# Optimization experiments

Measured on AMD Instinct MI355X. Metric: run time of the kernel, lower is better.

## Reference

```python
import jax, jax.numpy as jnp
import numpy as np
from jax import lax

B, C, H, W = 16, 512, 16, 300
K, G = 8, 2          # k_clusters, g_clusters (gvlad)
OUT = 5994           # n speakers
DN = ('NCHW', 'OIHW', 'NCHW')


def setup_inputs() -> dict:
    key = jax.random.key(0)
    ks = jax.random.split(key, 10)
    s = lambda fan: 1.0 / np.sqrt(fan)
    return {
        'x5': jax.random.normal(ks[0], (B, C, H, W), jnp.float32),
        'x4': jnp.zeros((1, 1, 1, 1), jnp.float32),
        'x3': jnp.zeros((1, 1, 1, 1), jnp.float32),
        'x2': jnp.zeros((1, 1, 1, 1), jnp.float32),
        'x1': jnp.zeros((1, 1, 1, 1), jnp.float32),
        'conv_w': jax.random.normal(ks[1], (C, C, 7, 1), jnp.float32) * s(C * 7),
        'conv_b': jnp.zeros((C,), jnp.float32),
        'cc_w': jax.random.normal(ks[2], (K + G, C, 7, 1), jnp.float32) * s(C * 7),
        'cc_b': jnp.zeros((K + G,), jnp.float32),
        'centroids': jax.random.normal(ks[3], (K + G, C), jnp.float32),
        'fc_w': jax.random.normal(ks[4], (C, C * K), jnp.float32) * s(C * K),
        'fc_b': jnp.zeros((C,), jnp.float32),
        'logit_w': jax.random.normal(ks[5], (OUT, C), jnp.float32) * s(C),
    }


def _conv(x, w, b=None):
    y = lax.conv_general_dilated(x, w, (1, 1), 'VALID', dimension_numbers=DN)
    if b is not None:
        y = y + b[None, :, None, None]
    return y


def _forward(x5, conv_w, conv_b, cc_w, cc_b, centroids, fc_w, fc_b, logit_w):
    feats = jnp.maximum(_conv(x5, conv_w, conv_b), 0.0)      # (B,C,H',W) relu conv
    scores = _conv(x5, cc_w, cc_b)                           # (B,K+G,H',W)
    assign = jax.nn.softmax(scores, axis=1)                  # soft cluster assignment
    # VLAD: sum_hw a[b,k,h,w]*(f[b,c,h,w] - cent[k,c]), computed without
    # materializing the (B,K+G,C,H',W) residual tensor (same math, fused form)
    agg = jnp.einsum('bkhw,bchw->bkc', assign, feats)        # (B,K+G,C)
    asum = jnp.sum(assign, axis=(2, 3))                      # (B,K+G)
    cluster_res = agg - asum[:, :, None] * centroids[None]   # (B,K+G,C)
    cluster_res = cluster_res[:, :K, :]                      # gvlad: drop ghost clusters
    norm = jnp.linalg.norm(cluster_res, axis=-1, keepdims=True)
    cluster_l2 = cluster_res / jnp.maximum(norm, 1e-12)
    vlad = cluster_l2.reshape(-1, K * C)                     # (B, K*C)
    emb = jnp.maximum(vlad @ fc_w.T + fc_b, 0.0)             # (B,C)
    logit = emb @ logit_w.T                                  # (B,OUT)
    return emb, logit


def reference(x5, x4, x3, x2, x1, conv_w, conv_b, cc_w, cc_b, centroids,
              fc_w, fc_b, logit_w):
    # x4..x1 are unused by Decoder.forward (only x5 flows through)
    return _forward(x5, conv_w, conv_b, cc_w, cc_b, centroids, fc_w, fc_b, logit_w)
```

## Files before the change

kernel.cpp:

```cpp
#include <hip/hip_runtime.h>
#include <hip/hip_bf16.h>

typedef __attribute__((ext_vector_type(8))) short bf16x8;
typedef __attribute__((ext_vector_type(4))) float f32x4;

__device__ __forceinline__ void async16(const void* g, void* l) {
    __builtin_amdgcn_global_load_lds(
        (const __attribute__((address_space(1))) unsigned int*)g,
        (__attribute__((address_space(3))) unsigned int*)l, 16, 0, 0);
}

__global__ __launch_bounds__(256) void pack_all(const float* __restrict__ x5,
                                                const float* __restrict__ conv_w,
                                                const float* __restrict__ cc_w,
                                                __hip_bfloat16* __restrict__ X3,
                                                __hip_bfloat16* __restrict__ A2f) {
    __shared__ __align__(16) float smem[64 * 65];
    const int f = blockIdx.x;
    if (f < 10240) {
        float(*tile)[65] = (float(*)[65])smem;
        const int ct = f / 1280, r = f % 1280;
        const int wt = r >> 8, bh = r & 255;
        const int b = bh >> 4, h = bh & 15;
        const int w0 = wt * 64, c0 = ct * 64;
        const int lw = (threadIdx.x & 15) * 4;
        const int lc = threadIdx.x >> 4;
#pragma unroll
        for (int i = 0; i < 4; ++i) {
            const int c = lc + i * 16;
            const int w = w0 + lw;
            const float* src = &x5[((size_t)(b * 512 + c0 + c) * 16 + h) * 300 + w];
            float4 v = {0.f, 0.f, 0.f, 0.f};
            if (w + 3 < 300) v = *(const float4*)src;
            else {
                if (w < 300)     v.x = src[0];
                if (w + 1 < 300) v.y = src[1];
                if (w + 2 < 300) v.z = src[2];
            }
            *(float4*)&tile[c][lw] = v;
        }
        __syncthreads();
        const int sc = (threadIdx.x & 7) * 8;
        const int sw0 = threadIdx.x >> 3;
#pragma unroll
        for (int i = 0; i < 2; ++i) {
            const int wl = sw0 + i * 32;
            const int w = w0 + wl;
            if (w < 300) {
                __hip_bfloat16 p[8];
#pragma unroll
                for (int j = 0; j < 8; ++j) p[j] = __float2bfloat16(tile[sc + j][wl]);
                *(uint4*)&X3[(((size_t)(b * 16 + h) * 300 + w)) * 512 + c0 + sc] = *(uint4*)p;
            }
        }
    } else {
        float* w = smem;
        const int co = f - 10240;
        if (co < 522) {
            const float4* src = (co < 512) ? (const float4*)(conv_w + (size_t)co * 3584)
                                           : (const float4*)(cc_w + (size_t)(co - 512) * 3584);
            for (int i = threadIdx.x; i < 896; i += 256) *(float4*)&w[i * 4] = src[i];
        } else {
            for (int i = threadIdx.x; i < 3584; i += 256) w[i] = 0.f;
        }
        __syncthreads();
        const int g = co >> 4, fl = co & 15;
        for (int chunk = threadIdx.x; chunk < 448; chunk += 256) {
            const int kk0 = chunk * 8;
            const int kt = kk0 >> 5, sq = (kk0 >> 3) & 3;
            __hip_bfloat16 p[8];
#pragma unroll
            for (int j = 0; j < 8; ++j) {
                const int k = kk0 + j;
                p[j] = __float2bfloat16(w[(k & 511) * 7 + (k >> 9)]);
            }
            char* dst = (char*)A2f + (((size_t)g * 112 + kt) * 64 + sq * 16 + fl) * 16;
            *(uint4*)dst = *(uint4*)p;
        }
    }
}

__global__ __launch_bounds__(256) void scores_gemm(
    const __hip_bfloat16* __restrict__ A2f, const __hip_bfloat16* __restrict__ X3,
    const float* __restrict__ cc_b, float* __restrict__ assign,
    float* __restrict__ asum_part, float* __restrict__ agg) {
    __shared__ float sred[4][4][4];
    const int tid = threadIdx.x;
    const int wv = tid >> 6;
    const int lane = tid & 63;
    const int fl = lane & 15;
    const int sq = lane >> 4;
    const int gid = blockIdx.x;
    const int xcd = gid & 7;
    const int j = gid >> 3;
    const int b = xcd * 2 + (j >= 48 ? 1 : 0);
    const int nt = j % 48;

    {
        const int base = gid * 107;
        for (int i = tid; i < 107; i += 256) {
            const int idx = base + i;
            if (idx < 81920) agg[idx] = 0.f;
        }
    }

    const int n = nt * 64 + wv * 16 + fl;
    const int nc = n > 2999 ? 2999 : n;
    const char* gB = (const char*)X3 + ((size_t)(b * 4800 + nc)) * 1024 + sq * 16;
    const char* Af = (const char*)A2f + (((size_t)32 * 112) << 10) + ((size_t)lane << 4);

    f32x4 acc = {};
#pragma unroll 4
    for (int kt = 0; kt < 112; ++kt) {
        const bf16x8 a  = *(const bf16x8*)(Af + ((size_t)kt << 10));
        const bf16x8 bv = *(const bf16x8*)(gB + (size_t)(kt >> 4) * 307200 + (size_t)(kt & 15) * 64);
        acc = __builtin_amdgcn_mfma_f32_16x16x32_bf16(a, bv, acc, 0, 0, 0);
    }

    float s[4];
#pragma unroll
    for (int r = 0; r < 4; ++r) {
        const int k = sq * 4 + r;
        s[r] = (k < 10) ? (acc[r] + cc_b[k]) : -1e30f;
    }
    float mx = fmaxf(fmaxf(s[0], s[1]), fmaxf(s[2], s[3]));
    mx = fmaxf(mx, __shfl_xor(mx, 16, 64));
    mx = fmaxf(mx, __shfl_xor(mx, 32, 64));
    float e[4], es = 0.f;
#pragma unroll
    for (int r = 0; r < 4; ++r) {
        e[r] = (sq * 4 + r < 10) ? __expf(s[r] - mx) : 0.f;
        es += e[r];
    }
    es += __shfl_xor(es, 16, 64);
    es += __shfl_xor(es, 32, 64);
    const float inv = 1.f / es;
    const bool nval = (n < 3000);
    float pa[4];
#pragma unroll
    for (int r = 0; r < 4; ++r) {
        const int k = sq * 4 + r;
        const float a = e[r] * inv;
        pa[r] = nval ? a : 0.f;
        if (nval && k < 10) assign[(size_t)(b * 10 + k) * 3000 + n] = a;
    }
#pragma unroll
    for (int off = 1; off < 16; off <<= 1)
#pragma unroll
        for (int r = 0; r < 4; ++r) pa[r] += __shfl_xor(pa[r], off, 64);
    if (fl == 0) {
#pragma unroll
        for (int r = 0; r < 4; ++r) sred[wv][sq][r] = pa[r];
    }
    __syncthreads();
    if (tid < 10)
        asum_part[(nt * 16 + b) * 10 + tid] =
            sred[0][tid >> 2][tid & 3] + sred[1][tid >> 2][tid & 3] +
            sred[2][tid >> 2][tid & 3] + sred[3][tid >> 2][tid & 3];
}

__global__ __launch_bounds__(256, 4) void conv_gemm(
    const __hip_bfloat16* __restrict__ A2f, const __hip_bfloat16* __restrict__ X3,
    const float* __restrict__ conv_b, const float* __restrict__ assign,
    float* __restrict__ agg) {
    __shared__ __align__(16) char lds[16384];
    const int tid = threadIdx.x;
    const int wv = tid >> 6;
    const int lane = tid & 63;

    const int gid = blockIdx.x;
    const int xcd = gid & 7;
    const int j = gid >> 3;
    const int nb = xcd * 48 + (j >> 2);
    const int m0 = (j & 3) * 128;
    const int b = nb / 24;
    const int nt = nb % 24;

    const int row0 = wv * 16 + (lane >> 2);
    const int kseg = (lane & 3) ^ ((lane >> 3) & 3);
    int n0 = nt * 128 + row0;      if (n0 > 2999) n0 = 2999;
    int n1 = nt * 128 + row0 + 64; if (n1 > 2999) n1 = 2999;
    const char* gB0 = (const char*)X3 + ((size_t)((b * 16 + n0 / 300) * 300 + n0 % 300)) * 1024 + (size_t)kseg * 16;
    const char* gB1 = (const char*)X3 + ((size_t)((b * 16 + n1 / 300) * 300 + n1 % 300)) * 1024 + (size_t)kseg * 16;
    char* lB = lds + wv * 1024 + lane * 16;

    const int wm = (wv & 1) * 64;
    const int wn = (wv >> 1) * 64;
    const int fl = lane & 15;
    const int sq = lane >> 4;
    int boff[4];
#pragma unroll
    for (int i = 0; i < 4; ++i) {
        const int swz = (sq ^ ((fl >> 1) & 3)) * 16;
        boff[i] = (wn + i * 16 + fl) * 64 + swz;
    }
    const char* Af = (const char*)A2f;
    const int gb = (m0 >> 4) + ((wv & 1) << 2);

    f32x4 acc[4][4] = {};
    bf16x8 aC[4], aN[4];

#define ISSUE_B(kt, ph)                                                                \
    {                                                                                  \
        const size_t badd = (size_t)((kt) >> 4) * 307200 + (size_t)((kt) & 15) * 64;   \
        async16(gB0 + badd, lB + (ph) * 8192);                                         \
        async16(gB1 + badd, lB + (ph) * 8192 + 4096);                                  \
    }
#define PRE_A(kt, arr)                                                                 \
    {                                                                                  \
        _Pragma("unroll")                                                              \
        for (int mi = 0; mi < 4; ++mi)                                                 \
            arr[mi] = *(const bf16x8*)(Af + (((size_t)(gb + mi) * 112 + (kt)) << 10) + (lane << 4)); \
    }
#define COMPUTE(ph, arr)                                                               \
    {                                                                                  \
        _Pragma("unroll")                                                              \
        for (int ni = 0; ni < 4; ++ni) {                                               \
            const bf16x8 bv = *(const bf16x8*)(lds + (ph) * 8192 + boff[ni]);          \
            _Pragma("unroll")                                                          \
            for (int mi = 0; mi < 4; ++mi)                                             \
                acc[mi][ni] = __builtin_amdgcn_mfma_f32_16x16x32_bf16(arr[mi], bv, acc[mi][ni], 0, 0, 0); \
        }                                                                              \
    }

    ISSUE_B(0, 0);
    PRE_A(0, aC);
    for (int kt = 0; kt < 112; kt += 2) {
        __syncthreads();
        ISSUE_B(kt + 1, 1);
        PRE_A(kt + 1, aN);
        COMPUTE(0, aC);
        __syncthreads();
        if (kt < 110) { ISSUE_B(kt + 2, 0); PRE_A(kt + 2, aC); }
        COMPUTE(1, aN);
    }
#undef ISSUE_B
#undef PRE_A
#undef COMPUTE

    const int quad4 = sq * 4;
#pragma unroll
    for (int mi = 0; mi < 4; ++mi) {
        const int cob = m0 + wm + mi * 16 + quad4;
        const float b0 = conv_b[cob + 0], b1 = conv_b[cob + 1],
                    b2 = conv_b[cob + 2], b3 = conv_b[cob + 3];
#pragma unroll
        for (int ni = 0; ni < 4; ++ni) {
            acc[mi][ni][0] = fmaxf(acc[mi][ni][0] + b0, 0.f);
            acc[mi][ni][1] = fmaxf(acc[mi][ni][1] + b1, 0.f);
            acc[mi][ni][2] = fmaxf(acc[mi][ni][2] + b2, 0.f);
            acc[mi][ni][3] = fmaxf(acc[mi][ni][3] + b3, 0.f);
        }
    }
    int nn[4];
#pragma unroll
    for (int ni = 0; ni < 4; ++ni) nn[ni] = nt * 128 + wn + ni * 16 + fl;
    const float* asg = assign + (size_t)b * 30000;
    const int s_ = ((fl & 1) << 3) | ((fl & 2) << 1) | ((fl & 4) >> 1) | ((fl & 8) >> 3);
    const int co_off = (s_ >> 2) * 16 + quad4 + (s_ & 3);
    float red10[10];
    for (int k = 0; k < 10; ++k) {
        float av[4];
#pragma unroll
        for (int ni = 0; ni < 4; ++ni)
            av[ni] = (nn[ni] < 3000) ? asg[(size_t)k * 3000 + nn[ni]] : 0.f;
        float part[16];
#pragma unroll
        for (int mi = 0; mi < 4; ++mi)
#pragma unroll
            for (int r = 0; r < 4; ++r)
                part[mi * 4 + r] = av[0] * acc[mi][0][r] + av[1] * acc[mi][1][r]
                                 + av[2] * acc[mi][2][r] + av[3] * acc[mi][3][r];
#pragma unroll
        for (int bit = 0; bit < 4; ++bit) {
            const int off = 1 << bit;
            const int h = 8 >> bit;
            const bool hi = (fl >> bit) & 1;
#pragma unroll
            for (int jj = 0; jj < h; ++jj) {
                const float mine = hi ? part[jj + h] : part[jj];
                const float send = hi ? part[jj] : part[jj + h];
                part[jj] = mine + __shfl_xor(send, off, 64);
            }
        }
        red10[k] = part[0];
    }
    float* sagg = (float*)lds;
    if (wv < 2) {
#pragma unroll
        for (int k = 0; k < 10; ++k) sagg[((wv * 10 + k) << 6) + co_off] = red10[k];
    }
    __syncthreads();
    if (wv >= 2) {
        const int wmh = wv & 1;
#pragma unroll
        for (int k = 0; k < 10; ++k) {
            const float v = red10[k] + sagg[((wmh * 10 + k) << 6) + co_off];
            atomicAdd(&agg[(size_t)(b * 10 + k) * 512 + m0 + wm + co_off], v);
        }
    }
}

__global__ __launch_bounds__(1024) void fc_fused(const float* __restrict__ agg,
                                                 const float* __restrict__ asum_part,
                                                 const float* __restrict__ centroids,
                                                 const float* __restrict__ fc_w,
                                                 const float* __restrict__ fc_b,
                                                 float* __restrict__ out) {
    __shared__ float res[4096];
    __shared__ float sasum[8];
    __shared__ float red2[16][4];
    __shared__ float scale[8];
    const int b = blockIdx.y;
    const int t = threadIdx.x;
    if (t < 8) {
        float s = 0.f;
#pragma unroll
        for (int p = 0; p < 48; ++p) s += asum_part[(p * 16 + b) * 10 + t];
        sasum[t] = s;
    }
    __syncthreads();
    const int b0 = t >> 9;
    float sqv[4] = {0.f, 0.f, 0.f, 0.f};
#pragma unroll
    for (int jj = 0; jj < 4; ++jj) {
        const int i = t + jj * 1024;
        const int k = b0 + jj * 2;
        const int c = i & 511;
        const float r = agg[(size_t)(b * 10 + k) * 512 + c] - sasum[k] * centroids[k * 512 + c];
        res[i] = r;
        sqv[jj] += r * r;
    }
    const int lane = t & 63, w = t >> 6;
#pragma unroll
    for (int jj = 0; jj < 4; ++jj) {
        float v = sqv[jj];
        for (int off = 32; off; off >>= 1) v += __shfl_xor(v, off, 64);
        if (lane == 0) red2[w][jj] = v;
    }
    __syncthreads();
    if (t < 8) {
        const int half = (t & 1) * 8;
        const int jj = t >> 1;
        float ss = 0.f;
#pragma unroll
        for (int i2 = 0; i2 < 8; ++i2) ss += red2[half + i2][jj];
        scale[t] = 1.f / fmaxf(sqrtf(ss), 1e-12f);
    }
    __syncthreads();

    const int col = t >> 5;
    const int ks = t & 31;
    const int co = blockIdx.x * 32 + col;
    const float4* w4 = (const float4*)(fc_w + (size_t)co * 4096);
    float acc = 0.f;
#pragma unroll 4
    for (int j2 = 0; j2 < 32; ++j2) {
        const int i = ks + 32 * j2;
        const float4 wv = w4[i];
        const float4 rv = *(const float4*)&res[i * 4];
        acc += (rv.x * wv.x + rv.y * wv.y + rv.z * wv.z + rv.w * wv.w) * scale[j2 >> 2];
    }
    acc += __shfl_down(acc, 16, 32);
    acc += __shfl_down(acc, 8, 32);
    acc += __shfl_down(acc, 4, 32);
    acc += __shfl_down(acc, 2, 32);
    acc += __shfl_down(acc, 1, 32);
    if (ks == 0) out[b * 512 + co] = fmaxf(acc + fc_b[co], 0.f);
}

__global__ __launch_bounds__(1024) void logit_kernel(const float* __restrict__ emb,
                                                     const float* __restrict__ logit_w,
                                                     float* __restrict__ out) {
    __shared__ float se[512];
    const int gid = blockIdx.x;
    const int xcd = gid & 7;
    const int j = gid >> 3;
    const int otile = xcd * 3 + (j >> 4);
    const int b = j & 15;
    if (threadIdx.x < 512) se[threadIdx.x] = emb[b * 512 + threadIdx.x];
    __syncthreads();
    const int ol = threadIdx.x >> 2;
    const int ks = threadIdx.x & 3;
    const int o = otile * 256 + ol;
    if (o < 5994) {
        const float4* w4 = (const float4*)(logit_w + (size_t)o * 512);
        float acc = 0.f;
#pragma unroll 8
        for (int j2 = 0; j2 < 32; ++j2) {
            const int i = ks + 4 * j2;
            const float4 w = w4[i];
            acc += w.x * se[4 * i] + w.y * se[4 * i + 1] + w.z * se[4 * i + 2] + w.w * se[4 * i + 3];
        }
        acc += __shfl_down(acc, 2, 4);
        acc += __shfl_down(acc, 1, 4);
        if (ks == 0) out[8192 + b * 5994 + o] = acc;
    }
}

extern "C" void kernel_launch(void* const* d_in, const int* in_sizes, int n_in,
                              void* d_out, int out_size, void* d_ws, size_t ws_size,
                              hipStream_t stream) {
    (void)in_sizes; (void)n_in; (void)out_size; (void)ws_size;
    const float* x5       = (const float*)d_in[0];
    const float* conv_w   = (const float*)d_in[5];
    const float* conv_b   = (const float*)d_in[6];
    const float* cc_w     = (const float*)d_in[7];
    const float* cc_b     = (const float*)d_in[8];
    const float* centroids= (const float*)d_in[9];
    const float* fc_w     = (const float*)d_in[10];
    const float* fc_b     = (const float*)d_in[11];
    const float* logit_w  = (const float*)d_in[12];
    float* out = (float*)d_out;

    char* ws = (char*)d_ws;
    __hip_bfloat16* X3  = (__hip_bfloat16*)(ws);
    __hip_bfloat16* A2f = (__hip_bfloat16*)(ws + 78643200);
    float* assign       = (float*)(ws + 83230720);
    float* asum_part    = (float*)(ws + 85150720);
    float* agg          = (float*)(ws + 85181440);

    pack_all<<<dim3(10880), 256, 0, stream>>>(x5, conv_w, cc_w, X3, A2f);
    scores_gemm<<<dim3(768), 256, 0, stream>>>(A2f, X3, cc_b, assign, asum_part, agg);
    conv_gemm<<<dim3(1536), 256, 0, stream>>>(A2f, X3, conv_b, assign, agg);
    fc_fused<<<dim3(16, 16), 1024, 0, stream>>>(agg, asum_part, centroids, fc_w, fc_b, out);
    logit_kernel<<<dim3(384), 1024, 0, stream>>>(out, logit_w, out);
}
```

Measured before the change: 537.3 us.

## Retile conv GEMM to 128x256 blocks with 8 waves and LDS-staged A

The conv GEMM now runs 512-thread blocks covering a 128x256 output tile instead of 256-thread 128x128 tiles. Each K step is 64 wide, and both A and B are staged into double-buffered LDS with async global-to-LDS loads, synchronised by explicit vmcnt waits and barriers. Compute phases are raised with s_setprio, and the epilogue reduces four waves' partials through LDS before the atomics. The aim is to halve redundant A fetches per output and deepen the pipeline. The cost is 96KB of LDS per block, which lowers occupancy to about one block per CU.

```diff
diff --git a/kernel.cpp b/kernel.cpp
--- a/kernel.cpp
+++ b/kernel.cpp
@@ -159,84 +159,132 @@
             sred[2][tid >> 2][tid & 3] + sred[3][tid >> 2][tid & 3];
 }
 
-__global__ __launch_bounds__(256, 4) void conv_gemm(
+__global__ __launch_bounds__(512) void conv_gemm(
     const __hip_bfloat16* __restrict__ A2f, const __hip_bfloat16* __restrict__ X3,
     const float* __restrict__ conv_b, const float* __restrict__ assign,
     float* __restrict__ agg) {
-    __shared__ __align__(16) char lds[16384];
+    __shared__ __align__(16) char lds[98304];
     const int tid = threadIdx.x;
     const int wv = tid >> 6;
     const int lane = tid & 63;
+    const int fl = lane & 15, sq = lane >> 4;
 
     const int gid = blockIdx.x;
     const int xcd = gid & 7;
     const int j = gid >> 3;
-    const int nb = xcd * 48 + (j >> 2);
+    const int u = xcd * 24 + (j >> 2);
     const int m0 = (j & 3) * 128;
-    const int b = nb / 24;
-    const int nt = nb % 24;
-
-    const int row0 = wv * 16 + (lane >> 2);
-    const int kseg = (lane & 3) ^ ((lane >> 3) & 3);
-    int n0 = nt * 128 + row0;      if (n0 > 2999) n0 = 2999;
-    int n1 = nt * 128 + row0 + 64; if (n1 > 2999) n1 = 2999;
-    const char* gB0 = (const char*)X3 + ((size_t)((b * 16 + n0 / 300) * 300 + n0 % 300)) * 1024 + (size_t)kseg * 16;
-    const char* gB1 = (const char*)X3 + ((size_t)((b * 16 + n1 / 300) * 300 + n1 % 300)) * 1024 + (size_t)kseg * 16;
-    char* lB = lds + wv * 1024 + lane * 16;
+    const int b = u / 12;
+    const int nt2 = u % 12;
+
+    const int l3 = lane >> 3, l7 = lane & 7;
+    const int sp = l7 ^ l3;
+    const char* srcB[4];
+#pragma unroll
+    for (int c = 0; c < 4; ++c) {
+        int n = nt2 * 256 + (wv * 4 + c) * 8 + l3;
+        if (n > 2999) n = 2999;
+        srcB[c] = (const char*)X3 + ((size_t)(b * 4800 + n)) * 1024
+                + (sp >> 2) * 64 + (sp & 3) * 16;
+    }
+    const int gbase = m0 >> 4;
+    const char* srcA[2];
+#pragma unroll
+    for (int c = 0; c < 2; ++c) {
+        const int ca = wv * 2 + c;
+        srcA[c] = (const char*)A2f + (((size_t)(gbase + (ca >> 1)) * 112 + (ca & 1)) << 10)
+                + ((size_t)lane << 4);
+    }
+    char* dstB = lds + (size_t)(wv * 4) * 1024 + ((size_t)lane << 4);
+    char* dstA = lds + 32768 + (size_t)(wv * 2) * 1024 + ((size_t)lane << 4);
 
     const int wm = (wv & 1) * 64;
     const int wn = (wv >> 1) * 64;
-    const int fl = lane & 15;
-    const int sq = lane >> 4;
-    int boff[4];
-#pragma unroll
-    for (int i = 0; i < 4; ++i) {
-        const int swz = (sq ^ ((fl >> 1) & 3)) * 16;
-        boff[i] = (wn + i * 16 + fl) * 64 + swz;
-    }
-    const char* Af = (const char*)A2f;
-    const int gb = (m0 >> 4) + ((wv & 1) << 2);
+    int bo_[4][2], ao_[4][2];
+#pragma unroll
+    for (int ni = 0; ni < 4; ++ni)
+#pragma unroll
+        for (int kk = 0; kk < 2; ++kk) {
+            const int r = wn + ni * 16 + fl;
+            bo_[ni][kk] = r * 128 + ((((kk * 4 + sq) ^ (fl & 7))) << 4);
+        }
+#pragma unroll
+    for (int mi = 0; mi < 4; ++mi)
+#pragma unroll
+        for (int kk = 0; kk < 2; ++kk)
+            ao_[mi][kk] = 32768 + (((((wv & 1) * 4 + mi) * 2) + kk) << 10) + (lane << 4);
 
     f32x4 acc[4][4] = {};
-    bf16x8 aC[4], aN[4];
-
-#define ISSUE_B(kt, ph)                                                                \
-    {                                                                                  \
-        const size_t badd = (size_t)((kt) >> 4) * 307200 + (size_t)((kt) & 15) * 64;   \
-        async16(gB0 + badd, lB + (ph) * 8192);                                         \
-        async16(gB1 + badd, lB + (ph) * 8192 + 4096);                                  \
-    }
-#define PRE_A(kt, arr)                                                                 \
-    {                                                                                  \
-        _Pragma("unroll")                                                              \
-        for (int mi = 0; mi < 4; ++mi)                                                 \
-            arr[mi] = *(const bf16x8*)(Af + (((size_t)(gb + mi) * 112 + (kt)) << 10) + (lane << 4)); \
-    }
-#define COMPUTE(ph, arr)                                                               \
-    {                                                                                  \
-        _Pragma("unroll")                                                              \
-        for (int ni = 0; ni < 4; ++ni) {                                               \
-            const bf16x8 bv = *(const bf16x8*)(lds + (ph) * 8192 + boff[ni]);          \
-            _Pragma("unroll")                                                          \
-            for (int mi = 0; mi < 4; ++mi)                                             \
-                acc[mi][ni] = __builtin_amdgcn_mfma_f32_16x16x32_bf16(arr[mi], bv, acc[mi][ni], 0, 0, 0); \
-        }                                                                              \
-    }
-
-    ISSUE_B(0, 0);
-    PRE_A(0, aC);
-    for (int kt = 0; kt < 112; kt += 2) {
-        __syncthreads();
-        ISSUE_B(kt + 1, 1);
-        PRE_A(kt + 1, aN);
-        COMPUTE(0, aC);
-        __syncthreads();
-        if (kt < 110) { ISSUE_B(kt + 2, 0); PRE_A(kt + 2, aC); }
-        COMPUTE(1, aN);
-    }
-#undef ISSUE_B
-#undef PRE_A
-#undef COMPUTE
+    bf16x8 aF[4][2], bF[2][2];
+
+#define STAGE(t, buf)                                                                \
+    {                                                                                \
+        const size_t bo = (size_t)((t) >> 3) * 307200 + (size_t)((t) & 7) * 128;     \
+        const size_t ao = (size_t)(t) << 11;                                         \
+        char* dB = dstB + (buf) * 49152;                                             \
+        char* dA = dstA + (buf) * 49152;                                             \
+        async16(srcB[0] + bo, dB);                                                   \
+        async16(srcB[1] + bo, dB + 1024);                                            \
+        async16(srcB[2] + bo, dB + 2048);                                            \
+        async16(srcB[3] + bo, dB + 3072);                                            \
+        async16(srcA[0] + ao, dA);                                                   \
+        async16(srcA[1] + ao, dA + 1024);                                            \
+    }
+#define BODY(t, buf, LAST)                                                           \
+    {                                                                                \
+        const char* Lb = lds + (buf) * 49152;                                        \
+        if (LAST) asm volatile("s_waitcnt vmcnt(0)" ::: "memory");                   \
+        else      asm volatile("s_waitcnt vmcnt(6)" ::: "memory");                   \
+        __builtin_amdgcn_s_barrier();                                                \
+        _Pragma("unroll")                                                            \
+        for (int mi = 0; mi < 4; ++mi) {                                             \
+            aF[mi][0] = *(const bf16x8*)(Lb + ao_[mi][0]);                           \
+            aF[mi][1] = *(const bf16x8*)(Lb + ao_[mi][1]);                           \
+        }                                                                            \
+        _Pragma("unroll")                                                            \
+        for (int ni = 0; ni < 2; ++ni) {                                             \
+            bF[ni][0] = *(const bf16x8*)(Lb + bo_[ni][0]);                           \
+            bF[ni][1] = *(const bf16x8*)(Lb + bo_[ni][1]);                           \
+        }                                                                            \
+        __builtin_amdgcn_s_barrier();                                                \
+        __builtin_amdgcn_s_setprio(1);                                               \
+        _Pragma("unroll")                                                            \
+        for (int ni = 0; ni < 2; ++ni)                                               \
+            _Pragma("unroll")                                                        \
+            for (int mi = 0; mi < 4; ++mi) {                                         \
+                acc[mi][ni] = __builtin_amdgcn_mfma_f32_16x16x32_bf16(aF[mi][0], bF[ni][0], acc[mi][ni], 0, 0, 0); \
+                acc[mi][ni] = __builtin_amdgcn_mfma_f32_16x16x32_bf16(aF[mi][1], bF[ni][1], acc[mi][ni], 0, 0, 0); \
+            }                                                                        \
+        __builtin_amdgcn_s_setprio(0);                                               \
+        __builtin_amdgcn_s_barrier();                                                \
+        _Pragma("unroll")                                                            \
+        for (int ni = 0; ni < 2; ++ni) {                                             \
+            bF[ni][0] = *(const bf16x8*)(Lb + bo_[ni + 2][0]);                       \
+            bF[ni][1] = *(const bf16x8*)(Lb + bo_[ni + 2][1]);                       \
+        }                                                                            \
+        __builtin_amdgcn_s_barrier();                                                \
+        __builtin_amdgcn_s_setprio(1);                                               \
+        _Pragma("unroll")                                                            \
+        for (int ni = 0; ni < 2; ++ni)                                               \
+            _Pragma("unroll")                                                        \
+            for (int mi = 0; mi < 4; ++mi) {                                         \
+                acc[mi][ni + 2] = __builtin_amdgcn_mfma_f32_16x16x32_bf16(aF[mi][0], bF[ni][0], acc[mi][ni + 2], 0, 0, 0); \
+                acc[mi][ni + 2] = __builtin_amdgcn_mfma_f32_16x16x32_bf16(aF[mi][1], bF[ni][1], acc[mi][ni + 2], 0, 0, 0); \
+            }                                                                        \
+        __builtin_amdgcn_s_setprio(0);                                               \
+        __builtin_amdgcn_s_barrier();                                                \
+    }
+
+    STAGE(0, 0);
+    STAGE(1, 1);
+    for (int t = 0; t < 55; ++t) {
+        const int buf = t & 1;
+        BODY(t, buf, false);
+        if (t < 54) STAGE(t + 2, buf);
+    }
+    BODY(55, 1, true);
+#undef STAGE
+#undef BODY
 
     const int quad4 = sq * 4;
 #pragma unroll
@@ -254,7 +302,7 @@
     }
     int nn[4];
 #pragma unroll
-    for (int ni = 0; ni < 4; ++ni) nn[ni] = nt * 128 + wn + ni * 16 + fl;
+    for (int ni = 0; ni < 4; ++ni) nn[ni] = nt2 * 256 + wn + ni * 16 + fl;
     const float* asg = assign + (size_t)b * 30000;
     const int s_ = ((fl & 1) << 3) | ((fl & 2) << 1) | ((fl & 4) >> 1) | ((fl & 8) >> 3);
     const int co_off = (s_ >> 2) * 16 + quad4 + (s_ & 3);
@@ -286,17 +334,18 @@
         red10[k] = part[0];
     }
     float* sagg = (float*)lds;
+    __syncthreads();
+#pragma unroll
+    for (int k = 0; k < 10; ++k) sagg[(wv * 10 + k) * 64 + co_off] = red10[k];
+    __syncthreads();
     if (wv < 2) {
 #pragma unroll
-        for (int k = 0; k < 10; ++k) sagg[((wv * 10 + k) << 6) + co_off] = red10[k];
-    }
-    __syncthreads();
-    if (wv >= 2) {
-        const int wmh = wv & 1;
-#pragma unroll
         for (int k = 0; k < 10; ++k) {
-            const float v = red10[k] + sagg[((wmh * 10 + k) << 6) + co_off];
-            atomicAdd(&agg[(size_t)(b * 10 + k) * 512 + m0 + wm + co_off], v);
+            const float v = sagg[((wv + 0) * 10 + k) * 64 + co_off]
+                          + sagg[((wv + 2) * 10 + k) * 64 + co_off]
+                          + sagg[((wv + 4) * 10 + k) * 64 + co_off]
+                          + sagg[((wv + 6) * 10 + k) * 64 + co_off];
+            atomicAdd(&agg[(size_t)(b * 10 + k) * 512 + m0 + wv * 64 + co_off], v);
         }
     }
 }
@@ -422,7 +471,7 @@
 
     pack_all<<<dim3(10880), 256, 0, stream>>>(x5, conv_w, cc_w, X3, A2f);
     scores_gemm<<<dim3(768), 256, 0, stream>>>(A2f, X3, cc_b, assign, asum_part, agg);
-    conv_gemm<<<dim3(1536), 256, 0, stream>>>(A2f, X3, conv_b, assign, agg);
+    conv_gemm<<<dim3(768), 512, 0, stream>>>(A2f, X3, conv_b, assign, agg);
     fc_fused<<<dim3(16, 16), 1024, 0, stream>>>(agg, asum_part, centroids, fc_w, fc_b, out);
     logit_kernel<<<dim3(384), 1024, 0, stream>>>(out, logit_w, out);
 }
```

Result: slower. 548.5 us (+2.1%).
